# Kernel optimization log

Hardware: AMD Instinct MI355X
Metric: run time of the kernel (lower is better)

## Reference

```python
import jax, jax.numpy as jnp
import numpy as np

# SmallViT config (reconstructed; see shape_source)
B, C, H, W = 1024, 3, 32, 32
P = 4                # patch size
D = 128              # embed dim
NH, DH = 4, 32       # heads, head dim
FF = 256             # mlp hidden
L = 4                # encoder layers
T = (H // P) * (W // P) + 1  # 65 tokens
NQ = 4               # qubits
EPS = 1e-5


def layer_norm(x, s, b):
    m = x.mean(-1, keepdims=True)
    v = ((x - m) ** 2).mean(-1, keepdims=True)
    return (x - m) * jax.lax.rsqrt(v + EPS) * s + b


def setup_inputs() -> dict:
    key = jax.random.key(0)
    ks = iter(jax.random.split(key, 32))
    w = lambda *shape: jax.random.normal(next(ks), shape, jnp.float32) * 0.02
    inp = {
        'x': jax.random.normal(next(ks), (B, C, H, W), jnp.float32),
        'patch_w': w(D, C, P, P),
        'patch_b': jnp.zeros((D,), jnp.float32),
        'cls_token': w(1, 1, D),
        'pos_embed': w(1, T, D),
        # stacked per-layer encoder params (torch Linear convention: [out,in])
        'qkv_w': w(L, 3 * D, D), 'qkv_b': jnp.zeros((L, 3 * D), jnp.float32),
        'out_w': w(L, D, D),     'out_b': jnp.zeros((L, D), jnp.float32),
        'ln1_s': jnp.ones((L, D), jnp.float32), 'ln1_b': jnp.zeros((L, D), jnp.float32),
        'ln2_s': jnp.ones((L, D), jnp.float32), 'ln2_b': jnp.zeros((L, D), jnp.float32),
        'ff1_w': w(L, FF, D), 'ff1_b': jnp.zeros((L, FF), jnp.float32),
        'ff2_w': w(L, D, FF), 'ff2_b': jnp.zeros((L, D), jnp.float32),
        # quantum_reduce: Linear(128,32) -> ReLU -> Linear(32,4)
        'qr1_w': w(32, D), 'qr1_b': jnp.zeros((32,), jnp.float32),
        'qr2_w': w(NQ, 32), 'qr2_b': jnp.zeros((NQ,), jnp.float32),
        'q_weights': jax.random.normal(next(ks), (NQ,), jnp.float32),
        'clf_w': w(10, D + NQ), 'clf_b': jnp.zeros((10,), jnp.float32),
    }
    return inp


def reference(x, patch_w, patch_b, cls_token, pos_embed,
              qkv_w, qkv_b, out_w, out_b, ln1_s, ln1_b, ln2_s, ln2_b,
              ff1_w, ff1_b, ff2_w, ff2_b,
              qr1_w, qr1_b, qr2_w, qr2_b, q_weights, clf_w, clf_b):
    b = x.shape[0]
    # patch embed: conv stride==kernel -> reshape + einsum
    xp = x.reshape(b, C, H // P, P, W // P, P)
    tok = jnp.einsum('bcipjq,dcpq->bijd', xp, patch_w).reshape(b, -1, D) + patch_b
    # prepend cls, add pos
    h = jnp.concatenate([jnp.broadcast_to(cls_token, (b, 1, D)), tok], axis=1) + pos_embed
    scale = 1.0 / np.sqrt(DH)
    for i in range(L):
        # self-attention (post-LN encoder layer)
        qkv = h @ qkv_w[i].T + qkv_b[i]                      # [b,T,3D]
        q, k, v = jnp.split(qkv, 3, axis=-1)
        q = q.reshape(b, T, NH, DH).transpose(0, 2, 1, 3)
        k = k.reshape(b, T, NH, DH).transpose(0, 2, 1, 3)
        v = v.reshape(b, T, NH, DH).transpose(0, 2, 1, 3)
        attn = jax.nn.softmax(jnp.einsum('bhqd,bhkd->bhqk', q, k) * scale, axis=-1)
        o = jnp.einsum('bhqk,bhkd->bhqd', attn, v).transpose(0, 2, 1, 3).reshape(b, T, D)
        o = o @ out_w[i].T + out_b[i]
        h = layer_norm(h + o, ln1_s[i], ln1_b[i])
        ff = jax.nn.relu(h @ ff1_w[i].T + ff1_b[i]) @ ff2_w[i].T + ff2_b[i]
        h = layer_norm(h + ff, ln2_s[i], ln2_b[i])
    cls_out = h[:, 0]                                         # [b,D]
    q_in = jnp.tanh(jax.nn.relu(cls_out @ qr1_w.T + qr1_b) @ qr2_w.T + qr2_b)  # [b,4]
    # closed-form 4-qubit circuit: RY(in) RX(w) + CNOT chain -> <Z_i> = cumprod cos(in)cos(w)
    q_out = jnp.cumprod(jnp.cos(q_in) * jnp.cos(q_weights)[None, :], axis=-1)
    combined = jnp.concatenate([cls_out, q_out], axis=1)      # [b,132]
    return combined @ clf_w.T + clf_b                         # [b,10]
```

## Files before the change

kernel.cpp:

```cpp
#include <hip/hip_runtime.h>

typedef unsigned short ushort_t;
typedef unsigned int   uint32;
typedef short s16x8 __attribute__((ext_vector_type(8)));
typedef float f32x4 __attribute__((ext_vector_type(4)));

#define HS    136
#define KOF   0
#define VOF   9248
#define SLOF  18464
#define BIGN  29344
#define EPS_  1e-5f
#define SCALE2_ 0.25503483f

#define MFMA16(a,b,c) __builtin_amdgcn_mfma_f32_16x16x32_bf16((a),(b),(c),0,0,0)

__device__ __forceinline__ float bfu(ushort_t u) {
  union { uint32 i; float f; } c; c.i = ((uint32)u) << 16; return c.f;
}
__device__ __forceinline__ void bf2(uint32 u, float& a, float& b) {
  union { uint32 i; float f; } c0, c1;
  c0.i = u << 16; c1.i = u & 0xffff0000u; a = c0.f; b = c1.f;
}
__device__ __forceinline__ ushort_t f2bf(float f) {
  union { float f; uint32 i; } c; c.f = f;
  uint32 r = c.i + 0x7fffu + ((c.i >> 16) & 1u);
  return (ushort_t)(r >> 16);
}

__device__ bool sniff_f32(const ushort_t* x) {
  int insane = 0, zeros = 0;
  for (int i = 0; i < 256; ++i) {
    ushort_t u = x[i];
    int e = (u >> 7) & 0xFF;
    if (u == 0) zeros++;
    else if (e == 0xFF || e < 0x60) insane++;
  }
  return (insane >= 16) || (zeros >= 64);
}

struct WPack {
  const void* src[23];
  unsigned    off[23];
  unsigned    n[23];
};

__global__ __launch_bounds__(256) void canon(WPack p, const ushort_t* x, ushort_t* dst,
                                             int* flagOut) {
  const bool f32 = sniff_f32(x);
  const int gid = blockIdx.x * blockDim.x + threadIdx.x;
  const int gsz = gridDim.x * blockDim.x;
  for (int a = 0; a < 23; ++a) {
    unsigned n = p.n[a];
    ushort_t* d = dst + p.off[a];
    if (f32) {
      const float* s = (const float*)p.src[a];
      for (unsigned i = gid; i < n; i += gsz) d[i] = f2bf(s[i]);
    } else {
      const ushort_t* s = (const ushort_t*)p.src[a];
      for (unsigned i = gid; i < n; i += gsz) d[i] = s[i];
    }
  }
  if (blockIdx.x == 0 && threadIdx.x == 0) *flagOut = f32 ? 1 : 0;
}

__global__ __launch_bounds__(320, 2)
void vit_fused(const ushort_t* __restrict__ x,
               const ushort_t* __restrict__ patch_w,
               const ushort_t* __restrict__ patch_b,
               const ushort_t* __restrict__ cls_token,
               const ushort_t* __restrict__ pos_embed,
               const ushort_t* __restrict__ qkv_w,
               const ushort_t* __restrict__ qkv_b,
               const ushort_t* __restrict__ out_w,
               const ushort_t* __restrict__ out_b,
               const ushort_t* __restrict__ ln1_s,
               const ushort_t* __restrict__ ln1_b,
               const ushort_t* __restrict__ ln2_s,
               const ushort_t* __restrict__ ln2_b,
               const ushort_t* __restrict__ ff1_w,
               const ushort_t* __restrict__ ff1_b,
               const ushort_t* __restrict__ ff2_w,
               const ushort_t* __restrict__ ff2_b,
               const ushort_t* __restrict__ qr1_w,
               const ushort_t* __restrict__ qr1_b,
               const ushort_t* __restrict__ qr2_w,
               const ushort_t* __restrict__ qr2_b,
               const ushort_t* __restrict__ q_weights,
               const ushort_t* __restrict__ clf_w,
               const ushort_t* __restrict__ clf_b,
               const int* __restrict__ flag,
               void* __restrict__ out)
{
  __shared__ __align__(16) ushort_t h_s[80 * HS];
  __shared__ __align__(16) ushort_t big[BIGN];

  const int tid  = threadIdx.x;
  const int wid  = tid >> 6;
  const int lane = tid & 63;
  const int lr   = lane & 15;
  const int lq   = lane >> 4;
  const int b    = blockIdx.x;
  const bool f32m = (*flag != 0);
  const int m0 = wid * 16;

  uint32* bx = (uint32*)big;
  if (f32m) {
    const float* xf = (const float*)x + (size_t)b * 3072;
    for (int i = tid; i < 1536; i += 320) {
      uint32 lo = f2bf(xf[2 * i]);
      uint32 hi = f2bf(xf[2 * i + 1]);
      bx[i] = lo | (hi << 16);
    }
  } else {
    const uint32* xb = (const uint32*)x + (size_t)b * 1536;
    for (int i = tid; i < 1536; i += 320) bx[i] = xb[i];
  }
  {
    const uint32* pw = (const uint32*)patch_w;
    for (int i = tid; i < 3072; i += 320) bx[1536 + i] = pw[i];
  }
  __syncthreads();

  #pragma unroll 1
  for (int idx = tid; idx < 8192; idx += 320) {
    int p = idx >> 7, d = idx & 127;
    int pi = p >> 3, pj = p & 7;
    float acc = 0.f;
    #pragma unroll
    for (int c = 0; c < 3; ++c) {
      #pragma unroll
      for (int py = 0; py < 4; ++py) {
        const uint32* xr = bx + ((c * 1024 + (pi * 4 + py) * 32 + pj * 4) >> 1);
        const uint32* wr = bx + 1536 + ((d * 48 + c * 16 + py * 4) >> 1);
        #pragma unroll
        for (int q2 = 0; q2 < 2; ++q2) {
          float xa, xb2, wa, wb;
          bf2(xr[q2], xa, xb2); bf2(wr[q2], wa, wb);
          acc += xa * wa + xb2 * wb;
        }
      }
    }
    acc += bfu(patch_b[d]) + bfu(pos_embed[(1 + p) * 128 + d]);
    h_s[(1 + p) * HS + d] = f2bf(acc);
  }
  if (tid < 128) h_s[tid] = f2bf(bfu(cls_token[tid]) + bfu(pos_embed[tid]));
  for (int i = tid; i < 15 * HS; i += 320) h_s[65 * HS + i] = 0;

  #pragma unroll 1
  for (int il = 0; il < 4; ++il) {
    __syncthreads();

    const ushort_t* Wqkv = qkv_w + (size_t)il * 384 * 128;
    const ushort_t* Bqkv = qkv_b + il * 384;
    const ushort_t* Wo   = out_w + (size_t)il * 128 * 128;
    ushort_t* bw = big + SLOF + wid * 2176;

    #pragma unroll 2
    for (int u = wid * 16; u < wid * 16 + 16; ++u) {
      int ty = u & 1, r = u >> 1;
      int mt = r >> 3, nt = r & 7;
      int km0 = mt * 16;
      int rb = (ty ? 256 : 128) + nt * 16;
      float bv = bfu(Bqkv[rb + lr]);
      f32x4 acc = {bv, bv, bv, bv};
      #pragma unroll
      for (int kc = 0; kc < 4; ++kc) {
        s16x8 a  = *(const s16x8*)&h_s[(km0 + lr) * HS + kc * 32 + lq * 8];
        s16x8 bb = *(const s16x8*)&Wqkv[(rb + lr) * 128 + kc * 32 + lq * 8];
        acc = MFMA16(a, bb, acc);
      }
      if (!ty) {
        #pragma unroll
        for (int i = 0; i < 4; ++i) {
          int row = km0 + lq * 4 + i;
          if (row < 68) big[KOF + row * 136 + nt * 16 + lr] = f2bf(acc[i]);
        }
      } else {
        int tk = km0 + lq * 4;
        if (tk < 68) {
          uint32 w0 = (uint32)f2bf(acc[0]) | ((uint32)f2bf(acc[1]) << 16);
          uint32 w1 = (uint32)f2bf(acc[2]) | ((uint32)f2bf(acc[3]) << 16);
          uint32* dst = (uint32*)&big[VOF + (nt * 16 + lr) * 72 + tk];
          dst[0] = w0; dst[1] = w1;
        }
      }
    }
    __syncthreads();

    {
      s16x8 ha[4];
      #pragma unroll
      for (int kc = 0; kc < 4; ++kc)
        ha[kc] = *(const s16x8*)&h_s[(m0 + lr) * HS + kc * 32 + lq * 8];
      f32x4 opA[8];
      #pragma unroll
      for (int nt = 0; nt < 8; ++nt) {
        float bv = bfu(out_b[il * 128 + nt * 16 + lr]);
        opA[nt] = (f32x4){bv, bv, bv, bv};
      }
      #pragma unroll 1
      for (int ih = 0; ih < 4; ++ih) {
        #pragma unroll
        for (int n2 = 0; n2 < 2; ++n2) {
          int rb = ih * 32 + n2 * 16;
          float bv = bfu(Bqkv[rb + lr]);
          f32x4 acc = {bv, bv, bv, bv};
          #pragma unroll
          for (int kc = 0; kc < 4; ++kc) {
            s16x8 bb = *(const s16x8*)&Wqkv[(rb + lr) * 128 + kc * 32 + lq * 8];
            acc = MFMA16(ha[kc], bb, acc);
          }
          #pragma unroll
          for (int i = 0; i < 4; ++i)
            bw[(lq * 4 + i) * 40 + n2 * 16 + lr] = f2bf(acc[i] * SCALE2_);
        }
        s16x8 aq = *(const s16x8*)&bw[lr * 40 + lq * 8];
        f32x4 S[5];
        #pragma unroll
        for (int jt = 0; jt < 5; ++jt) {
          s16x8 bb = *(const s16x8*)&big[KOF + (jt * 16 + lr) * 136 + ih * 32 + lq * 8];
          f32x4 z = {0.f, 0.f, 0.f, 0.f};
          S[jt] = MFMA16(aq, bb, z);
        }
        float mx[4] = {-1e30f, -1e30f, -1e30f, -1e30f};
        #pragma unroll
        for (int jt = 0; jt < 5; ++jt)
          #pragma unroll
          for (int i = 0; i < 4; ++i) {
            float sv = S[jt][i];
            if (jt == 4 && lr > 0) sv = -1e30f;
            S[jt][i] = sv;
            mx[i] = fmaxf(mx[i], sv);
          }
        #pragma unroll
        for (int off = 1; off < 16; off <<= 1)
          #pragma unroll
          for (int i = 0; i < 4; ++i) mx[i] = fmaxf(mx[i], __shfl_xor(mx[i], off));
        float sm[4] = {0.f, 0.f, 0.f, 0.f};
        #pragma unroll
        for (int jt = 0; jt < 5; ++jt)
          #pragma unroll
          for (int i = 0; i < 4; ++i) {
            float pv = exp2f(S[jt][i] - mx[i]);
            S[jt][i] = pv; sm[i] += pv;
          }
        #pragma unroll
        for (int off = 1; off < 16; off <<= 1)
          #pragma unroll
          for (int i = 0; i < 4; ++i) sm[i] += __shfl_xor(sm[i], off);
        float inv[4];
        #pragma unroll
        for (int i = 0; i < 4; ++i) inv[i] = 1.f / sm[i];
        #pragma unroll
        for (int i = 0; i < 4; ++i)
          #pragma unroll
          for (int jt = 0; jt < 4; ++jt)
            bw[(lq * 4 + i) * 72 + jt * 16 + lr] = f2bf(S[jt][i] * inv[i]);
        f32x4 ov[2];
        #pragma unroll
        for (int n2 = 0; n2 < 2; ++n2) {
          f32x4 acc = {0.f, 0.f, 0.f, 0.f};
          #pragma unroll
          for (int kc = 0; kc < 2; ++kc) {
            s16x8 a  = *(const s16x8*)&bw[lr * 72 + kc * 32 + lq * 8];
            s16x8 bb = *(const s16x8*)&big[VOF + (ih * 32 + n2 * 16 + lr) * 72 + kc * 32 + lq * 8];
            acc = MFMA16(a, bb, acc);
          }
          float v64 = bfu(big[VOF + (ih * 32 + n2 * 16 + lr) * 72 + 64]);
          #pragma unroll
          for (int i = 0; i < 4; ++i) {
            float p64 = __shfl(S[4][i], lane & 48) * inv[i];
            acc[i] += p64 * v64;
          }
          ov[n2] = acc;
        }
        #pragma unroll
        for (int n2 = 0; n2 < 2; ++n2)
          #pragma unroll
          for (int i = 0; i < 4; ++i)
            bw[(lq * 4 + i) * 40 + n2 * 16 + lr] = f2bf(ov[n2][i]);
        s16x8 ao = *(const s16x8*)&bw[lr * 40 + lq * 8];
        #pragma unroll
        for (int nt = 0; nt < 8; ++nt) {
          s16x8 bb = *(const s16x8*)&Wo[(nt * 16 + lr) * 128 + ih * 32 + lq * 8];
          opA[nt] = MFMA16(ao, bb, opA[nt]);
        }
      }

      float sv[4] = {0, 0, 0, 0}, ssv[4] = {0, 0, 0, 0};
      #pragma unroll
      for (int nt = 0; nt < 8; ++nt)
        #pragma unroll
        for (int i = 0; i < 4; ++i) {
          float r = opA[nt][i] + bfu(h_s[(m0 + lq * 4 + i) * HS + nt * 16 + lr]);
          opA[nt][i] = r; sv[i] += r; ssv[i] += r * r;
        }
      #pragma unroll
      for (int off = 1; off < 16; off <<= 1)
        #pragma unroll
        for (int i = 0; i < 4; ++i) {
          sv[i]  += __shfl_xor(sv[i], off);
          ssv[i] += __shfl_xor(ssv[i], off);
        }
      float mean[4], inv2[4];
      #pragma unroll
      for (int i = 0; i < 4; ++i) {
        mean[i] = sv[i] * (1.f / 128.f);
        inv2[i] = rsqrtf(fmaxf(ssv[i] * (1.f / 128.f) - mean[i] * mean[i], 0.f) + EPS_);
      }
      #pragma unroll
      for (int nt = 0; nt < 8; ++nt) {
        float g  = bfu(ln1_s[il * 128 + nt * 16 + lr]);
        float be = bfu(ln1_b[il * 128 + nt * 16 + lr]);
        #pragma unroll
        for (int i = 0; i < 4; ++i)
          h_s[(m0 + lq * 4 + i) * HS + nt * 16 + lr] =
              f2bf((opA[nt][i] - mean[i]) * inv2[i] * g + be);
      }

      const ushort_t* W1 = ff1_w + (size_t)il * 256 * 128;
      const ushort_t* W2 = ff2_w + (size_t)il * 128 * 256;
      s16x8 hf[4];
      #pragma unroll
      for (int kc = 0; kc < 4; ++kc)
        hf[kc] = *(const s16x8*)&h_s[(m0 + lr) * HS + kc * 32 + lq * 8];
      f32x4 acc2[8];
      #pragma unroll
      for (int nt = 0; nt < 8; ++nt) {
        float bv = bfu(ff2_b[il * 128 + nt * 16 + lr]);
        acc2[nt] = (f32x4){bv, bv, bv, bv};
      }
      #pragma unroll 1
      for (int half = 0; half < 2; ++half) {
        #pragma unroll 2
        for (int n8 = 0; n8 < 8; ++n8) {
          int ng = half * 8 + n8;
          float bv = bfu(ff1_b[il * 256 + ng * 16 + lr]);
          f32x4 acc = {bv, bv, bv, bv};
          #pragma unroll
          for (int kc = 0; kc < 4; ++kc) {
            s16x8 bb = *(const s16x8*)&W1[(ng * 16 + lr) * 128 + kc * 32 + lq * 8];
            acc = MFMA16(hf[kc], bb, acc);
          }
          #pragma unroll
          for (int i = 0; i < 4; ++i)
            bw[(lq * 4 + i) * 136 + n8 * 16 + lr] = f2bf(fmaxf(acc[i], 0.f));
        }
        #pragma unroll
        for (int kc = 0; kc < 4; ++kc) {
          s16x8 a2 = *(const s16x8*)&bw[lr * 136 + kc * 32 + lq * 8];
          #pragma unroll
          for (int nt = 0; nt < 8; ++nt) {
            s16x8 bb = *(const s16x8*)&W2[(nt * 16 + lr) * 256 + half * 128 + kc * 32 + lq * 8];
            acc2[nt] = MFMA16(a2, bb, acc2[nt]);
          }
        }
      }
      float s2[4] = {0, 0, 0, 0}, ss2[4] = {0, 0, 0, 0};
      #pragma unroll
      for (int nt = 0; nt < 8; ++nt)
        #pragma unroll
        for (int i = 0; i < 4; ++i) {
          float r = acc2[nt][i] + bfu(h_s[(m0 + lq * 4 + i) * HS + nt * 16 + lr]);
          acc2[nt][i] = r; s2[i] += r; ss2[i] += r * r;
        }
      #pragma unroll
      for (int off = 1; off < 16; off <<= 1)
        #pragma unroll
        for (int i = 0; i < 4; ++i) {
          s2[i]  += __shfl_xor(s2[i], off);
          ss2[i] += __shfl_xor(ss2[i], off);
        }
      float mean2[4], invb[4];
      #pragma unroll
      for (int i = 0; i < 4; ++i) {
        mean2[i] = s2[i] * (1.f / 128.f);
        invb[i]  = rsqrtf(fmaxf(ss2[i] * (1.f / 128.f) - mean2[i] * mean2[i], 0.f) + EPS_);
      }
      #pragma unroll
      for (int nt = 0; nt < 8; ++nt) {
        float g  = bfu(ln2_s[il * 128 + nt * 16 + lr]);
        float be = bfu(ln2_b[il * 128 + nt * 16 + lr]);
        #pragma unroll
        for (int i = 0; i < 4; ++i)
          h_s[(m0 + lq * 4 + i) * HS + nt * 16 + lr] =
              f2bf((acc2[nt][i] - mean2[i]) * invb[i] * g + be);
      }
    }
  }

  __syncthreads();
  float* scr = (float*)big;
  {
    int j = tid & 31;
    const uint32* hrow0 = (const uint32*)h_s;
    const uint32* w = (const uint32*)qr1_w + j * 64;
    float acc = 0.f;
    #pragma unroll 4
    for (int k2 = 0; k2 < 64; ++k2) {
      float ha, hb, wa, wb;
      bf2(hrow0[k2], ha, hb); bf2(w[k2], wa, wb);
      acc += ha * wa + hb * wb;
    }
    float u = fmaxf(acc + bfu(qr1_b[j]), 0.f);
    if (tid < 32) scr[tid] = u;
  }
  __syncthreads();
  if (tid < 10) {
    float qo[4]; float cp = 1.f;
    #pragma unroll
    for (int j2 = 0; j2 < 4; ++j2) {
      float acc = 0.f;
      #pragma unroll
      for (int k = 0; k < 32; ++k) acc += scr[k] * bfu(qr2_w[j2 * 32 + k]);
      float qin = tanhf(acc + bfu(qr2_b[j2]));
      cp *= cosf(qin) * cosf(bfu(q_weights[j2]));
      qo[j2] = cp;
    }
    const uint32* hrow0 = (const uint32*)h_s;
    const uint32* cw = (const uint32*)clf_w + tid * 66;
    float acc = 0.f;
    #pragma unroll 4
    for (int k2 = 0; k2 < 64; ++k2) {
      float ha, hb, wa, wb;
      bf2(hrow0[k2], ha, hb); bf2(cw[k2], wa, wb);
      acc += ha * wa + hb * wb;
    }
    #pragma unroll
    for (int d = 0; d < 4; ++d) acc += qo[d] * bfu(clf_w[tid * 132 + 128 + d]);
    acc += bfu(clf_b[tid]);
    if (f32m) ((float*)out)[b * 10 + tid] = acc;
    else      ((ushort_t*)out)[b * 10 + tid] = f2bf(acc);
  }
}

extern "C" void kernel_launch(void* const* d_in, const int* in_sizes, int n_in,
                              void* d_out, int out_size, void* d_ws, size_t ws_size,
                              hipStream_t stream) {
  WPack p;
  unsigned cur = 0;
  for (int i = 0; i < 23; ++i) {
    p.src[i] = d_in[i + 1];
    p.off[i] = cur;
    p.n[i]   = (unsigned)in_sizes[i + 1];
    cur += (p.n[i] + 7u) & ~7u;
  }
  ushort_t* wsb = (ushort_t*)d_ws;
  unsigned flag_off = (cur * 2 + 3u) & ~3u;
  int* flagp = (int*)((char*)d_ws + flag_off);
  const ushort_t* x = (const ushort_t*)d_in[0];

  canon<<<dim3(128), dim3(256), 0, stream>>>(p, x, wsb, flagp);

  int B = out_size / 10;
  vit_fused<<<dim3(B), dim3(320), 0, stream>>>(
      x,
      wsb + p.off[0],  wsb + p.off[1],  wsb + p.off[2],  wsb + p.off[3],
      wsb + p.off[4],  wsb + p.off[5],  wsb + p.off[6],  wsb + p.off[7],
      wsb + p.off[8],  wsb + p.off[9],  wsb + p.off[10], wsb + p.off[11],
      wsb + p.off[12], wsb + p.off[13], wsb + p.off[14], wsb + p.off[15],
      wsb + p.off[16], wsb + p.off[17], wsb + p.off[18], wsb + p.off[19],
      wsb + p.off[20], wsb + p.off[21], wsb + p.off[22],
      flagp, d_out);
}
```

Baseline: 874.5 us.

## Split heads and FFN hidden across wave pairs with 640-thread blocks

Doubles the block from 5 to 10 waves. Each pair of waves shares one 16-row token tile: one wave handles heads 0-1 and FFN hidden half 0, the other handles heads 2-3 and hidden half 1. The second wave's partial out-projection and FF2 sums go through a new fp32 LDS exchange buffer and are added during the layernorm. This shortens the serial per-wave chain and raises the number of waves per CU. In exchange it needs more LDS (lower block occupancy), two extra barriers per layer, and leaves half the waves idle during the layernorms.

Measured after the change: 908.2 us. 3.9% more time.

```diff
diff --git a/kernel.cpp b/kernel.cpp
--- a/kernel.cpp
+++ b/kernel.cpp
@@ -9,7 +9,8 @@
 #define KOF   0
 #define VOF   9248
 #define SLOF  18464
-#define BIGN  29344
+#define EXOF  40224
+#define BIGN  61024
 #define EPS_  1e-5f
 #define SCALE2_ 0.25503483f
 
@@ -64,7 +65,7 @@
   if (blockIdx.x == 0 && threadIdx.x == 0) *flagOut = f32 ? 1 : 0;
 }
 
-__global__ __launch_bounds__(320, 2)
+__global__ __launch_bounds__(640, 3)
 void vit_fused(const ushort_t* __restrict__ x,
                const ushort_t* __restrict__ patch_w,
                const ushort_t* __restrict__ patch_b,
@@ -102,28 +103,33 @@
   const int lq   = lane >> 4;
   const int b    = blockIdx.x;
   const bool f32m = (*flag != 0);
-  const int m0 = wid * 16;
+  const int mt   = wid >> 1;
+  const int hg   = wid & 1;
+  const int m0   = mt * 16;
+
+  ushort_t* bw  = big + SLOF + wid * 2176;
+  float*    exf = (float*)&big[EXOF] + mt * 2080;
 
   uint32* bx = (uint32*)big;
   if (f32m) {
     const float* xf = (const float*)x + (size_t)b * 3072;
-    for (int i = tid; i < 1536; i += 320) {
+    for (int i = tid; i < 1536; i += 640) {
       uint32 lo = f2bf(xf[2 * i]);
       uint32 hi = f2bf(xf[2 * i + 1]);
       bx[i] = lo | (hi << 16);
     }
   } else {
     const uint32* xb = (const uint32*)x + (size_t)b * 1536;
-    for (int i = tid; i < 1536; i += 320) bx[i] = xb[i];
+    for (int i = tid; i < 1536; i += 640) bx[i] = xb[i];
   }
   {
     const uint32* pw = (const uint32*)patch_w;
-    for (int i = tid; i < 3072; i += 320) bx[1536 + i] = pw[i];
+    for (int i = tid; i < 3072; i += 640) bx[1536 + i] = pw[i];
   }
   __syncthreads();
 
   #pragma unroll 1
-  for (int idx = tid; idx < 8192; idx += 320) {
+  for (int idx = tid; idx < 8192; idx += 640) {
     int p = idx >> 7, d = idx & 127;
     int pi = p >> 3, pj = p & 7;
     float acc = 0.f;
@@ -145,7 +151,7 @@
     h_s[(1 + p) * HS + d] = f2bf(acc);
   }
   if (tid < 128) h_s[tid] = f2bf(bfu(cls_token[tid]) + bfu(pos_embed[tid]));
-  for (int i = tid; i < 15 * HS; i += 320) h_s[65 * HS + i] = 0;
+  for (int i = tid; i < 15 * HS; i += 640) h_s[65 * HS + i] = 0;
 
   #pragma unroll 1
   for (int il = 0; il < 4; ++il) {
@@ -154,13 +160,12 @@
     const ushort_t* Wqkv = qkv_w + (size_t)il * 384 * 128;
     const ushort_t* Bqkv = qkv_b + il * 384;
     const ushort_t* Wo   = out_w + (size_t)il * 128 * 128;
-    ushort_t* bw = big + SLOF + wid * 2176;
 
     #pragma unroll 2
-    for (int u = wid * 16; u < wid * 16 + 16; ++u) {
+    for (int u = wid * 8; u < wid * 8 + 8; ++u) {
       int ty = u & 1, r = u >> 1;
-      int mt = r >> 3, nt = r & 7;
-      int km0 = mt * 16;
+      int kmt = r >> 3, nt = r & 7;
+      int km0 = kmt * 16;
       int rb = (ty ? 256 : 128) + nt * 16;
       float bv = bfu(Bqkv[rb + lr]);
       f32x4 acc = {bv, bv, bv, bv};
@@ -188,19 +193,20 @@
     }
     __syncthreads();
 
+    f32x4 opA[8];
+    #pragma unroll
+    for (int nt = 0; nt < 8; ++nt) {
+      float bv = (hg == 0) ? bfu(out_b[il * 128 + nt * 16 + lr]) : 0.f;
+      opA[nt] = (f32x4){bv, bv, bv, bv};
+    }
     {
       s16x8 ha[4];
       #pragma unroll
       for (int kc = 0; kc < 4; ++kc)
         ha[kc] = *(const s16x8*)&h_s[(m0 + lr) * HS + kc * 32 + lq * 8];
-      f32x4 opA[8];
-      #pragma unroll
-      for (int nt = 0; nt < 8; ++nt) {
-        float bv = bfu(out_b[il * 128 + nt * 16 + lr]);
-        opA[nt] = (f32x4){bv, bv, bv, bv};
-      }
       #pragma unroll 1
-      for (int ih = 0; ih < 4; ++ih) {
+      for (int hh = 0; hh < 2; ++hh) {
+        int ih = hg * 2 + hh;
         #pragma unroll
         for (int n2 = 0; n2 < 2; ++n2) {
           int rb = ih * 32 + n2 * 16;
@@ -287,13 +293,23 @@
           opA[nt] = MFMA16(ao, bb, opA[nt]);
         }
       }
-
+    }
+    if (hg == 1) {
+      #pragma unroll
+      for (int nt = 0; nt < 8; ++nt)
+        #pragma unroll
+        for (int i = 0; i < 4; ++i)
+          exf[(lq * 4 + i) * 130 + nt * 16 + lr] = opA[nt][i];
+    }
+    __syncthreads();
+    if (hg == 0) {
       float sv[4] = {0, 0, 0, 0}, ssv[4] = {0, 0, 0, 0};
       #pragma unroll
       for (int nt = 0; nt < 8; ++nt)
         #pragma unroll
         for (int i = 0; i < 4; ++i) {
-          float r = opA[nt][i] + bfu(h_s[(m0 + lq * 4 + i) * HS + nt * 16 + lr]);
+          float r = opA[nt][i] + exf[(lq * 4 + i) * 130 + nt * 16 + lr]
+                  + bfu(h_s[(m0 + lq * 4 + i) * HS + nt * 16 + lr]);
           opA[nt][i] = r; sv[i] += r; ssv[i] += r * r;
         }
       #pragma unroll
@@ -303,22 +319,22 @@
           sv[i]  += __shfl_xor(sv[i], off);
           ssv[i] += __shfl_xor(ssv[i], off);
         }
-      float mean[4], inv2[4];
-      #pragma unroll
-      for (int i = 0; i < 4; ++i) {
-        mean[i] = sv[i] * (1.f / 128.f);
-        inv2[i] = rsqrtf(fmaxf(ssv[i] * (1.f / 128.f) - mean[i] * mean[i], 0.f) + EPS_);
-      }
       #pragma unroll
       for (int nt = 0; nt < 8; ++nt) {
         float g  = bfu(ln1_s[il * 128 + nt * 16 + lr]);
         float be = bfu(ln1_b[il * 128 + nt * 16 + lr]);
         #pragma unroll
-        for (int i = 0; i < 4; ++i)
+        for (int i = 0; i < 4; ++i) {
+          float mean = sv[i] * (1.f / 128.f);
+          float iv   = rsqrtf(fmaxf(ssv[i] * (1.f / 128.f) - mean * mean, 0.f) + EPS_);
           h_s[(m0 + lq * 4 + i) * HS + nt * 16 + lr] =
-              f2bf((opA[nt][i] - mean[i]) * inv2[i] * g + be);
-      }
-
+              f2bf((opA[nt][i] - mean) * iv * g + be);
+        }
+      }
+    }
+    __syncthreads();
+
+    {
       const ushort_t* W1 = ff1_w + (size_t)il * 256 * 128;
       const ushort_t* W2 = ff2_w + (size_t)il * 128 * 256;
       s16x8 hf[4];
@@ -328,64 +344,69 @@
       f32x4 acc2[8];
       #pragma unroll
       for (int nt = 0; nt < 8; ++nt) {
-        float bv = bfu(ff2_b[il * 128 + nt * 16 + lr]);
+        float bv = (hg == 0) ? bfu(ff2_b[il * 128 + nt * 16 + lr]) : 0.f;
         acc2[nt] = (f32x4){bv, bv, bv, bv};
       }
-      #pragma unroll 1
-      for (int half = 0; half < 2; ++half) {
-        #pragma unroll 2
-        for (int n8 = 0; n8 < 8; ++n8) {
-          int ng = half * 8 + n8;
-          float bv = bfu(ff1_b[il * 256 + ng * 16 + lr]);
-          f32x4 acc = {bv, bv, bv, bv};
-          #pragma unroll
-          for (int kc = 0; kc < 4; ++kc) {
-            s16x8 bb = *(const s16x8*)&W1[(ng * 16 + lr) * 128 + kc * 32 + lq * 8];
-            acc = MFMA16(hf[kc], bb, acc);
-          }
+      #pragma unroll 2
+      for (int n8 = 0; n8 < 8; ++n8) {
+        int ng = hg * 8 + n8;
+        float bv = bfu(ff1_b[il * 256 + ng * 16 + lr]);
+        f32x4 acc = {bv, bv, bv, bv};
+        #pragma unroll
+        for (int kc = 0; kc < 4; ++kc) {
+          s16x8 bb = *(const s16x8*)&W1[(ng * 16 + lr) * 128 + kc * 32 + lq * 8];
+          acc = MFMA16(hf[kc], bb, acc);
+        }
+        #pragma unroll
+        for (int i = 0; i < 4; ++i)
+          bw[(lq * 4 + i) * 136 + n8 * 16 + lr] = f2bf(fmaxf(acc[i], 0.f));
+      }
+      #pragma unroll
+      for (int kc = 0; kc < 4; ++kc) {
+        s16x8 a2 = *(const s16x8*)&bw[lr * 136 + kc * 32 + lq * 8];
+        #pragma unroll
+        for (int nt = 0; nt < 8; ++nt) {
+          s16x8 bb = *(const s16x8*)&W2[(nt * 16 + lr) * 256 + hg * 128 + kc * 32 + lq * 8];
+          acc2[nt] = MFMA16(a2, bb, acc2[nt]);
+        }
+      }
+      if (hg == 1) {
+        #pragma unroll
+        for (int nt = 0; nt < 8; ++nt)
           #pragma unroll
           for (int i = 0; i < 4; ++i)
-            bw[(lq * 4 + i) * 136 + n8 * 16 + lr] = f2bf(fmaxf(acc[i], 0.f));
-        }
-        #pragma unroll
-        for (int kc = 0; kc < 4; ++kc) {
-          s16x8 a2 = *(const s16x8*)&bw[lr * 136 + kc * 32 + lq * 8];
-          #pragma unroll
-          for (int nt = 0; nt < 8; ++nt) {
-            s16x8 bb = *(const s16x8*)&W2[(nt * 16 + lr) * 256 + half * 128 + kc * 32 + lq * 8];
-            acc2[nt] = MFMA16(a2, bb, acc2[nt]);
-          }
-        }
-      }
-      float s2[4] = {0, 0, 0, 0}, ss2[4] = {0, 0, 0, 0};
-      #pragma unroll
-      for (int nt = 0; nt < 8; ++nt)
-        #pragma unroll
-        for (int i = 0; i < 4; ++i) {
-          float r = acc2[nt][i] + bfu(h_s[(m0 + lq * 4 + i) * HS + nt * 16 + lr]);
-          acc2[nt][i] = r; s2[i] += r; ss2[i] += r * r;
-        }
-      #pragma unroll
-      for (int off = 1; off < 16; off <<= 1)
-        #pragma unroll
-        for (int i = 0; i < 4; ++i) {
-          s2[i]  += __shfl_xor(s2[i], off);
-          ss2[i] += __shfl_xor(ss2[i], off);
-        }
-      float mean2[4], invb[4];
-      #pragma unroll
-      for (int i = 0; i < 4; ++i) {
-        mean2[i] = s2[i] * (1.f / 128.f);
-        invb[i]  = rsqrtf(fmaxf(ss2[i] * (1.f / 128.f) - mean2[i] * mean2[i], 0.f) + EPS_);
-      }
-      #pragma unroll
-      for (int nt = 0; nt < 8; ++nt) {
-        float g  = bfu(ln2_s[il * 128 + nt * 16 + lr]);
-        float be = bfu(ln2_b[il * 128 + nt * 16 + lr]);
-        #pragma unroll
-        for (int i = 0; i < 4; ++i)
-          h_s[(m0 + lq * 4 + i) * HS + nt * 16 + lr] =
-              f2bf((acc2[nt][i] - mean2[i]) * invb[i] * g + be);
+            exf[(lq * 4 + i) * 130 + nt * 16 + lr] = acc2[nt][i];
+      }
+      __syncthreads();
+      if (hg == 0) {
+        float sv[4] = {0, 0, 0, 0}, ssv[4] = {0, 0, 0, 0};
+        #pragma unroll
+        for (int nt = 0; nt < 8; ++nt)
+          #pragma unroll
+          for (int i = 0; i < 4; ++i) {
+            float r = acc2[nt][i] + exf[(lq * 4 + i) * 130 + nt * 16 + lr]
+                    + bfu(h_s[(m0 + lq * 4 + i) * HS + nt * 16 + lr]);
+            acc2[nt][i] = r; sv[i] += r; ssv[i] += r * r;
+          }
+        #pragma unroll
+        for (int off = 1; off < 16; off <<= 1)
+          #pragma unroll
+          for (int i = 0; i < 4; ++i) {
+            sv[i]  += __shfl_xor(sv[i], off);
+            ssv[i] += __shfl_xor(ssv[i], off);
+          }
+        #pragma unroll
+        for (int nt = 0; nt < 8; ++nt) {
+          float g  = bfu(ln2_s[il * 128 + nt * 16 + lr]);
+          float be = bfu(ln2_b[il * 128 + nt * 16 + lr]);
+          #pragma unroll
+          for (int i = 0; i < 4; ++i) {
+            float mean = sv[i] * (1.f / 128.f);
+            float iv   = rsqrtf(fmaxf(ssv[i] * (1.f / 128.f) - mean * mean, 0.f) + EPS_);
+            h_s[(m0 + lq * 4 + i) * HS + nt * 16 + lr] =
+                f2bf((acc2[nt][i] - mean) * iv * g + be);
+          }
+        }
       }
     }
   }
@@ -454,7 +475,7 @@
   canon<<<dim3(128), dim3(256), 0, stream>>>(p, x, wsb, flagp);
 
   int B = out_size / 10;
-  vit_fused<<<dim3(B), dim3(320), 0, stream>>>(
+  vit_fused<<<dim3(B), dim3(640), 0, stream>>>(
       x,
       wsb + p.off[0],  wsb + p.off[1],  wsb + p.off[2],  wsb + p.off[3],
       wsb + p.off[4],  wsb + p.off[5],  wsb + p.off[6],  wsb + p.off[7],
```

## Split fused per-image ViT kernel into per-stage batched GEMM kernels

Applied to the files above, without the earlier changes.

Replaces the single per-image fused kernel with a pipeline of separate kernels for patch embed, QKV projection, attention, output projection with LayerNorm, FF1 and FF2 with LayerNorm, and the head. Intermediate activations now go through workspace buffers in global memory. Each GEMM tiles 64 rows across images, and weights are staged in shared memory once per block, so per-block weight reloads and the low occupancy of the large monolithic block go away. In exchange it adds many launches and extra global memory traffic for the intermediates. The old fused kernel is kept as a fallback when the workspace is too small or B is not a multiple of 64.

Result: faster. 724.3 us (-17.2%).

```diff
diff --git a/kernel.cpp b/kernel.cpp
--- a/kernel.cpp
+++ b/kernel.cpp
@@ -5,14 +5,8 @@
 typedef short s16x8 __attribute__((ext_vector_type(8)));
 typedef float f32x4 __attribute__((ext_vector_type(4)));
 
-#define HS    136
-#define KOF   0
-#define VOF   9248
-#define SLOF  18464
-#define BIGN  29344
 #define EPS_  1e-5f
 #define SCALE2_ 0.25503483f
-
 #define MFMA16(a,b,c) __builtin_amdgcn_mfma_f32_16x16x32_bf16((a),(b),(c),0,0,0)
 
 __device__ __forceinline__ float bfu(ushort_t u) {
@@ -64,46 +58,443 @@
   if (blockIdx.x == 0 && threadIdx.x == 0) *flagOut = f32 ? 1 : 0;
 }
 
+
+__global__ __launch_bounds__(256)
+void k_patch(const ushort_t* __restrict__ x, const ushort_t* __restrict__ patch_w,
+             const ushort_t* __restrict__ patch_b, const ushort_t* __restrict__ cls_token,
+             const ushort_t* __restrict__ pos_embed, const int* __restrict__ flag,
+             ushort_t* __restrict__ hbuf) {
+  __shared__ uint32 bx[4608];
+  const int tid = threadIdx.x, b = blockIdx.x;
+  const bool f32m = (*flag != 0);
+  if (f32m) {
+    const float* xf = (const float*)x + (size_t)b * 3072;
+    for (int i = tid; i < 1536; i += 256) {
+      uint32 lo = f2bf(xf[2 * i]);
+      uint32 hi = f2bf(xf[2 * i + 1]);
+      bx[i] = lo | (hi << 16);
+    }
+  } else {
+    const uint32* xb = (const uint32*)x + (size_t)b * 1536;
+    for (int i = tid; i < 1536; i += 256) bx[i] = xb[i];
+  }
+  {
+    const uint32* pw = (const uint32*)patch_w;
+    for (int i = tid; i < 3072; i += 256) bx[1536 + i] = pw[i];
+  }
+  __syncthreads();
+  #pragma unroll 1
+  for (int it = 0; it < 32; ++it) {
+    int idx = tid + 256 * it;
+    int p = idx >> 7, d = idx & 127;
+    int pi = p >> 3, pj = p & 7;
+    float acc = 0.f;
+    #pragma unroll
+    for (int c = 0; c < 3; ++c)
+      #pragma unroll
+      for (int py = 0; py < 4; ++py) {
+        const uint32* xr = bx + ((c * 1024 + (pi * 4 + py) * 32 + pj * 4) >> 1);
+        const uint32* wr = bx + 1536 + ((d * 48 + c * 16 + py * 4) >> 1);
+        #pragma unroll
+        for (int q2 = 0; q2 < 2; ++q2) {
+          float xa, xb2, wa, wb;
+          bf2(xr[q2], xa, xb2); bf2(wr[q2], wa, wb);
+          acc += xa * wa + xb2 * wb;
+        }
+      }
+    acc += bfu(patch_b[d]) + bfu(pos_embed[(1 + p) * 128 + d]);
+    hbuf[((size_t)b * 65 + 1 + p) * 128 + d] = f2bf(acc);
+  }
+  if (tid < 128)
+    hbuf[(size_t)b * 65 * 128 + tid] = f2bf(bfu(cls_token[tid]) + bfu(pos_embed[tid]));
+}
+
+__global__ __launch_bounds__(256)
+void k_qkv(const ushort_t* __restrict__ hbuf, const ushort_t* __restrict__ W,
+           const ushort_t* __restrict__ bias, ushort_t* __restrict__ qb,
+           ushort_t* __restrict__ kb, ushort_t* __restrict__ vtb) {
+  __shared__ __align__(16) ushort_t Bs[64 * 136];
+  const int tid = threadIdx.x, wid = tid >> 6, lane = tid & 63;
+  const int lr = lane & 15, lq = lane >> 4;
+  const int bm = blockIdx.x, nc = blockIdx.y;
+  {
+    const uint32* Wd = (const uint32*)W;
+    uint32* Bd = (uint32*)Bs;
+    for (int i = tid; i < 4096; i += 256) {
+      int row = i >> 6, cw = i & 63;
+      Bd[row * 68 + cw] = Wd[(nc * 64 + row) * 64 + cw];
+    }
+  }
+  __syncthreads();
+  const int r0 = bm * 64 + wid * 16;
+  s16x8 a[4];
+  #pragma unroll
+  for (int kc = 0; kc < 4; ++kc)
+    a[kc] = *(const s16x8*)&hbuf[(size_t)(r0 + lr) * 128 + kc * 32 + lq * 8];
+  #pragma unroll
+  for (int nt = 0; nt < 4; ++nt) {
+    int c0 = nc * 64 + nt * 16;
+    float bv = bfu(bias[c0 + lr]);
+    f32x4 acc = {bv, bv, bv, bv};
+    #pragma unroll
+    for (int kc = 0; kc < 4; ++kc) {
+      s16x8 bb = *(const s16x8*)&Bs[(nt * 16 + lr) * 136 + kc * 32 + lq * 8];
+      acc = MFMA16(a[kc], bb, acc);
+    }
+    int c = c0 + lr;
+    #pragma unroll
+    for (int i = 0; i < 4; ++i) {
+      int r = r0 + lq * 4 + i;
+      int b = r / 65, t = r - b * 65;
+      if (c0 < 128) {
+        int h = c >> 5, d = c & 31;
+        qb[((size_t)(b * 4 + h) * 80 + t) * 32 + d] = f2bf(acc[i] * SCALE2_);
+      } else if (c0 < 256) {
+        int c2 = c - 128;
+        kb[((size_t)(b * 4 + (c2 >> 5)) * 80 + t) * 32 + (c2 & 31)] = f2bf(acc[i]);
+      } else {
+        int c2 = c - 256;
+        vtb[((size_t)(b * 4 + (c2 >> 5)) * 32 + (c2 & 31)) * 80 + t] = f2bf(acc[i]);
+      }
+    }
+  }
+}
+
+__global__ __launch_bounds__(64)
+void k_attn(const ushort_t* __restrict__ qb, const ushort_t* __restrict__ kb,
+            const ushort_t* __restrict__ vtb, ushort_t* __restrict__ obuf) {
+  __shared__ __align__(16) ushort_t ks[80 * 40];
+  __shared__ __align__(16) ushort_t vs[32 * 96];
+  __shared__ __align__(16) ushort_t ps[16 * 96];
+  const int lane = threadIdx.x;
+  const int lr = lane & 15, lq = lane >> 4;
+  const int bh = blockIdx.x;
+  {
+    const uint32* kd = (const uint32*)(kb + (size_t)bh * 2560);
+    uint32* kls = (uint32*)ks;
+    #pragma unroll
+    for (int it = 0; it < 20; ++it) {
+      int u = it * 64 + lane;
+      kls[(u >> 4) * 20 + (u & 15)] = kd[u];
+    }
+    const uint32* vd = (const uint32*)(vtb + (size_t)bh * 2560);
+    uint32* vls = (uint32*)vs;
+    #pragma unroll
+    for (int it = 0; it < 20; ++it) {
+      int u = it * 64 + lane;
+      vls[(u / 40) * 48 + (u % 40)] = vd[u];
+    }
+    for (int u = lane; u < 512; u += 64)
+      vs[(u >> 4) * 96 + 80 + (u & 15)] = 0;
+  }
+  __syncthreads();
+  const int b = bh >> 2, h = bh & 3;
+  #pragma unroll 1
+  for (int mt = 0; mt < 5; ++mt) {
+    s16x8 aq = *(const s16x8*)&qb[((size_t)bh * 80 + mt * 16 + lr) * 32 + lq * 8];
+    f32x4 S[5];
+    #pragma unroll
+    for (int jt = 0; jt < 5; ++jt) {
+      s16x8 bb = *(const s16x8*)&ks[(jt * 16 + lr) * 40 + lq * 8];
+      f32x4 z = {0.f, 0.f, 0.f, 0.f};
+      S[jt] = MFMA16(aq, bb, z);
+    }
+    float mx[4] = {-1e30f, -1e30f, -1e30f, -1e30f};
+    #pragma unroll
+    for (int jt = 0; jt < 5; ++jt)
+      #pragma unroll
+      for (int i = 0; i < 4; ++i) {
+        float sv = S[jt][i];
+        if (jt == 4 && lr > 0) sv = -1e30f;
+        S[jt][i] = sv;
+        mx[i] = fmaxf(mx[i], sv);
+      }
+    #pragma unroll
+    for (int off = 1; off < 16; off <<= 1)
+      #pragma unroll
+      for (int i = 0; i < 4; ++i) mx[i] = fmaxf(mx[i], __shfl_xor(mx[i], off));
+    float sm[4] = {0.f, 0.f, 0.f, 0.f};
+    #pragma unroll
+    for (int jt = 0; jt < 5; ++jt)
+      #pragma unroll
+      for (int i = 0; i < 4; ++i) {
+        float pv = exp2f(S[jt][i] - mx[i]);
+        S[jt][i] = pv; sm[i] += pv;
+      }
+    #pragma unroll
+    for (int off = 1; off < 16; off <<= 1)
+      #pragma unroll
+      for (int i = 0; i < 4; ++i) sm[i] += __shfl_xor(sm[i], off);
+    float inv[4];
+    #pragma unroll
+    for (int i = 0; i < 4; ++i) inv[i] = 1.f / sm[i];
+    #pragma unroll
+    for (int i = 0; i < 4; ++i) {
+      #pragma unroll
+      for (int jt = 0; jt < 5; ++jt)
+        ps[(lq * 4 + i) * 96 + jt * 16 + lr] = f2bf(S[jt][i] * inv[i]);
+      ps[(lq * 4 + i) * 96 + 80 + lr] = 0;
+    }
+    #pragma unroll
+    for (int n2 = 0; n2 < 2; ++n2) {
+      f32x4 acc = {0.f, 0.f, 0.f, 0.f};
+      #pragma unroll
+      for (int kc = 0; kc < 3; ++kc) {
+        s16x8 a  = *(const s16x8*)&ps[lr * 96 + kc * 32 + lq * 8];
+        s16x8 bb = *(const s16x8*)&vs[(n2 * 16 + lr) * 96 + kc * 32 + lq * 8];
+        acc = MFMA16(a, bb, acc);
+      }
+      #pragma unroll
+      for (int i = 0; i < 4; ++i) {
+        int t = mt * 16 + lq * 4 + i;
+        if (t < 65)
+          obuf[((size_t)b * 65 + t) * 128 + h * 32 + n2 * 16 + lr] = f2bf(acc[i]);
+      }
+    }
+  }
+}
+
+__global__ __launch_bounds__(256)
+void k_out_ln(const ushort_t* __restrict__ obuf, const ushort_t* __restrict__ Wo,
+              const ushort_t* __restrict__ ob, const ushort_t* __restrict__ g,
+              const ushort_t* __restrict__ be, ushort_t* __restrict__ hbuf) {
+  __shared__ __align__(16) ushort_t Bs[128 * 136];
+  const int tid = threadIdx.x, wid = tid >> 6, lane = tid & 63;
+  const int lr = lane & 15, lq = lane >> 4;
+  const int bm = blockIdx.x;
+  {
+    const uint32* Wd = (const uint32*)Wo;
+    uint32* Bd = (uint32*)Bs;
+    for (int i = tid; i < 8192; i += 256)
+      Bd[(i >> 6) * 68 + (i & 63)] = Wd[i];
+  }
+  __syncthreads();
+  const int r0 = bm * 64 + wid * 16;
+  s16x8 a[4];
+  #pragma unroll
+  for (int kc = 0; kc < 4; ++kc)
+    a[kc] = *(const s16x8*)&obuf[(size_t)(r0 + lr) * 128 + kc * 32 + lq * 8];
+  float xr[8][4];
+  float sv[4] = {0, 0, 0, 0}, ssv[4] = {0, 0, 0, 0};
+  #pragma unroll
+  for (int nt = 0; nt < 8; ++nt) {
+    float bv = bfu(ob[nt * 16 + lr]);
+    f32x4 acc = {bv, bv, bv, bv};
+    #pragma unroll
+    for (int kc = 0; kc < 4; ++kc) {
+      s16x8 bb = *(const s16x8*)&Bs[(nt * 16 + lr) * 136 + kc * 32 + lq * 8];
+      acc = MFMA16(a[kc], bb, acc);
+    }
+    #pragma unroll
+    for (int i = 0; i < 4; ++i) {
+      float r = acc[i] + bfu(hbuf[(size_t)(r0 + lq * 4 + i) * 128 + nt * 16 + lr]);
+      xr[nt][i] = r; sv[i] += r; ssv[i] += r * r;
+    }
+  }
+  #pragma unroll
+  for (int off = 1; off < 16; off <<= 1)
+    #pragma unroll
+    for (int i = 0; i < 4; ++i) {
+      sv[i]  += __shfl_xor(sv[i], off);
+      ssv[i] += __shfl_xor(ssv[i], off);
+    }
+  #pragma unroll
+  for (int nt = 0; nt < 8; ++nt) {
+    float gg = bfu(g[nt * 16 + lr]);
+    float bb = bfu(be[nt * 16 + lr]);
+    #pragma unroll
+    for (int i = 0; i < 4; ++i) {
+      float mean = sv[i] * (1.f / 128.f);
+      float iv = rsqrtf(fmaxf(ssv[i] * (1.f / 128.f) - mean * mean, 0.f) + EPS_);
+      hbuf[(size_t)(r0 + lq * 4 + i) * 128 + nt * 16 + lr] =
+          f2bf((xr[nt][i] - mean) * iv * gg + bb);
+    }
+  }
+}
+
+__global__ __launch_bounds__(256)
+void k_ff1(const ushort_t* __restrict__ hbuf, const ushort_t* __restrict__ W1,
+           const ushort_t* __restrict__ b1, ushort_t* __restrict__ fbuf) {
+  __shared__ __align__(16) ushort_t Bs[64 * 136];
+  const int tid = threadIdx.x, wid = tid >> 6, lane = tid & 63;
+  const int lr = lane & 15, lq = lane >> 4;
+  const int bm = blockIdx.x, nc = blockIdx.y;
+  {
+    const uint32* Wd = (const uint32*)W1;
+    uint32* Bd = (uint32*)Bs;
+    for (int i = tid; i < 4096; i += 256) {
+      int row = i >> 6, cw = i & 63;
+      Bd[row * 68 + cw] = Wd[(nc * 64 + row) * 64 + cw];
+    }
+  }
+  __syncthreads();
+  const int r0 = bm * 64 + wid * 16;
+  s16x8 a[4];
+  #pragma unroll
+  for (int kc = 0; kc < 4; ++kc)
+    a[kc] = *(const s16x8*)&hbuf[(size_t)(r0 + lr) * 128 + kc * 32 + lq * 8];
+  #pragma unroll
+  for (int nt = 0; nt < 4; ++nt) {
+    int c0 = nc * 64 + nt * 16;
+    float bv = bfu(b1[c0 + lr]);
+    f32x4 acc = {bv, bv, bv, bv};
+    #pragma unroll
+    for (int kc = 0; kc < 4; ++kc) {
+      s16x8 bb = *(const s16x8*)&Bs[(nt * 16 + lr) * 136 + kc * 32 + lq * 8];
+      acc = MFMA16(a[kc], bb, acc);
+    }
+    #pragma unroll
+    for (int i = 0; i < 4; ++i)
+      fbuf[(size_t)(r0 + lq * 4 + i) * 256 + c0 + lr] = f2bf(fmaxf(acc[i], 0.f));
+  }
+}
+
+__global__ __launch_bounds__(256)
+void k_ff2_ln(const ushort_t* __restrict__ fbuf, const ushort_t* __restrict__ W2,
+              const ushort_t* __restrict__ b2, const ushort_t* __restrict__ g,
+              const ushort_t* __restrict__ be, ushort_t* __restrict__ hbuf) {
+  __shared__ __align__(16) ushort_t Bs[128 * 136];
+  const int tid = threadIdx.x, wid = tid >> 6, lane = tid & 63;
+  const int lr = lane & 15, lq = lane >> 4;
+  const int bm = blockIdx.x;
+  const int r0 = bm * 64 + wid * 16;
+  f32x4 acc2[8];
+  #pragma unroll
+  for (int nt = 0; nt < 8; ++nt) {
+    float bv = bfu(b2[nt * 16 + lr]);
+    acc2[nt] = (f32x4){bv, bv, bv, bv};
+  }
+  #pragma unroll 1
+  for (int half = 0; half < 2; ++half) {
+    {
+      const uint32* Wd = (const uint32*)W2;
+      uint32* Bd = (uint32*)Bs;
+      for (int i = tid; i < 8192; i += 256) {
+        int row = i >> 6, cw = i & 63;
+        Bd[row * 68 + cw] = Wd[row * 128 + half * 64 + cw];
+      }
+    }
+    __syncthreads();
+    s16x8 a[4];
+    #pragma unroll
+    for (int kc = 0; kc < 4; ++kc)
+      a[kc] = *(const s16x8*)&fbuf[(size_t)(r0 + lr) * 256 + half * 128 + kc * 32 + lq * 8];
+    #pragma unroll
+    for (int nt = 0; nt < 8; ++nt)
+      #pragma unroll
+      for (int kc = 0; kc < 4; ++kc) {
+        s16x8 bb = *(const s16x8*)&Bs[(nt * 16 + lr) * 136 + kc * 32 + lq * 8];
+        acc2[nt] = MFMA16(a[kc], bb, acc2[nt]);
+      }
+    __syncthreads();
+  }
+  float sv[4] = {0, 0, 0, 0}, ssv[4] = {0, 0, 0, 0};
+  #pragma unroll
+  for (int nt = 0; nt < 8; ++nt)
+    #pragma unroll
+    for (int i = 0; i < 4; ++i) {
+      float r = acc2[nt][i] + bfu(hbuf[(size_t)(r0 + lq * 4 + i) * 128 + nt * 16 + lr]);
+      acc2[nt][i] = r; sv[i] += r; ssv[i] += r * r;
+    }
+  #pragma unroll
+  for (int off = 1; off < 16; off <<= 1)
+    #pragma unroll
+    for (int i = 0; i < 4; ++i) {
+      sv[i]  += __shfl_xor(sv[i], off);
+      ssv[i] += __shfl_xor(ssv[i], off);
+    }
+  #pragma unroll
+  for (int nt = 0; nt < 8; ++nt) {
+    float gg = bfu(g[nt * 16 + lr]);
+    float bb = bfu(be[nt * 16 + lr]);
+    #pragma unroll
+    for (int i = 0; i < 4; ++i) {
+      float mean = sv[i] * (1.f / 128.f);
+      float iv = rsqrtf(fmaxf(ssv[i] * (1.f / 128.f) - mean * mean, 0.f) + EPS_);
+      hbuf[(size_t)(r0 + lq * 4 + i) * 128 + nt * 16 + lr] =
+          f2bf((acc2[nt][i] - mean) * iv * gg + bb);
+    }
+  }
+}
+
+__global__ __launch_bounds__(64)
+void k_head(const ushort_t* __restrict__ hbuf, const ushort_t* __restrict__ qr1_w,
+            const ushort_t* __restrict__ qr1_b, const ushort_t* __restrict__ qr2_w,
+            const ushort_t* __restrict__ qr2_b, const ushort_t* __restrict__ q_weights,
+            const ushort_t* __restrict__ clf_w, const ushort_t* __restrict__ clf_b,
+            const int* __restrict__ flag, void* __restrict__ out) {
+  __shared__ float scr[32];
+  const int lane = threadIdx.x, b = blockIdx.x;
+  const bool f32m = (*flag != 0);
+  const uint32* hrow0 = (const uint32*)(hbuf + (size_t)b * 65 * 128);
+  {
+    int j = lane & 31;
+    const uint32* w = (const uint32*)qr1_w + j * 64;
+    float acc = 0.f;
+    #pragma unroll 4
+    for (int k2 = 0; k2 < 64; ++k2) {
+      float ha, hb, wa, wb;
+      bf2(hrow0[k2], ha, hb); bf2(w[k2], wa, wb);
+      acc += ha * wa + hb * wb;
+    }
+    if (lane < 32) scr[lane] = fmaxf(acc + bfu(qr1_b[j]), 0.f);
+  }
+  __syncthreads();
+  if (lane < 10) {
+    float qo[4]; float cp = 1.f;
+    #pragma unroll
+    for (int j2 = 0; j2 < 4; ++j2) {
+      float acc = 0.f;
+      #pragma unroll
+      for (int k = 0; k < 32; ++k) acc += scr[k] * bfu(qr2_w[j2 * 32 + k]);
+      float qin = tanhf(acc + bfu(qr2_b[j2]));
+      cp *= cosf(qin) * cosf(bfu(q_weights[j2]));
+      qo[j2] = cp;
+    }
+    const uint32* cw = (const uint32*)clf_w + lane * 66;
+    float acc = 0.f;
+    #pragma unroll 4
+    for (int k2 = 0; k2 < 64; ++k2) {
+      float ha, hb, wa, wb;
+      bf2(hrow0[k2], ha, hb); bf2(cw[k2], wa, wb);
+      acc += ha * wa + hb * wb;
+    }
+    #pragma unroll
+    for (int d = 0; d < 4; ++d) acc += qo[d] * bfu(clf_w[lane * 132 + 128 + d]);
+    acc += bfu(clf_b[lane]);
+    if (f32m) ((float*)out)[b * 10 + lane] = acc;
+    else      ((ushort_t*)out)[b * 10 + lane] = f2bf(acc);
+  }
+}
+
+#define HS    136
+#define KOF   0
+#define VOF   9248
+#define SLOF  18464
+#define BIGN  29344
+
 __global__ __launch_bounds__(320, 2)
-void vit_fused(const ushort_t* __restrict__ x,
-               const ushort_t* __restrict__ patch_w,
-               const ushort_t* __restrict__ patch_b,
-               const ushort_t* __restrict__ cls_token,
-               const ushort_t* __restrict__ pos_embed,
-               const ushort_t* __restrict__ qkv_w,
-               const ushort_t* __restrict__ qkv_b,
-               const ushort_t* __restrict__ out_w,
-               const ushort_t* __restrict__ out_b,
-               const ushort_t* __restrict__ ln1_s,
-               const ushort_t* __restrict__ ln1_b,
-               const ushort_t* __restrict__ ln2_s,
-               const ushort_t* __restrict__ ln2_b,
-               const ushort_t* __restrict__ ff1_w,
-               const ushort_t* __restrict__ ff1_b,
-               const ushort_t* __restrict__ ff2_w,
-               const ushort_t* __restrict__ ff2_b,
-               const ushort_t* __restrict__ qr1_w,
-               const ushort_t* __restrict__ qr1_b,
-               const ushort_t* __restrict__ qr2_w,
-               const ushort_t* __restrict__ qr2_b,
-               const ushort_t* __restrict__ q_weights,
-               const ushort_t* __restrict__ clf_w,
-               const ushort_t* __restrict__ clf_b,
-               const int* __restrict__ flag,
-               void* __restrict__ out)
+void vit_mono(const ushort_t* __restrict__ x, const ushort_t* __restrict__ patch_w,
+              const ushort_t* __restrict__ patch_b, const ushort_t* __restrict__ cls_token,
+              const ushort_t* __restrict__ pos_embed, const ushort_t* __restrict__ qkv_w,
+              const ushort_t* __restrict__ qkv_b, const ushort_t* __restrict__ out_w,
+              const ushort_t* __restrict__ out_b, const ushort_t* __restrict__ ln1_s,
+              const ushort_t* __restrict__ ln1_b, const ushort_t* __restrict__ ln2_s,
+              const ushort_t* __restrict__ ln2_b, const ushort_t* __restrict__ ff1_w,
+              const ushort_t* __restrict__ ff1_b, const ushort_t* __restrict__ ff2_w,
+              const ushort_t* __restrict__ ff2_b, const ushort_t* __restrict__ qr1_w,
+              const ushort_t* __restrict__ qr1_b, const ushort_t* __restrict__ qr2_w,
+              const ushort_t* __restrict__ qr2_b, const ushort_t* __restrict__ q_weights,
+              const ushort_t* __restrict__ clf_w, const ushort_t* __restrict__ clf_b,
+              const int* __restrict__ flag, void* __restrict__ out)
 {
   __shared__ __align__(16) ushort_t h_s[80 * HS];
   __shared__ __align__(16) ushort_t big[BIGN];
-
-  const int tid  = threadIdx.x;
-  const int wid  = tid >> 6;
-  const int lane = tid & 63;
-  const int lr   = lane & 15;
-  const int lq   = lane >> 4;
-  const int b    = blockIdx.x;
+  const int tid = threadIdx.x, wid = tid >> 6, lane = tid & 63;
+  const int lr = lane & 15, lq = lane >> 4;
+  const int b = blockIdx.x;
   const bool f32m = (*flag != 0);
   const int m0 = wid * 16;
-
   uint32* bx = (uint32*)big;
   if (f32m) {
     const float* xf = (const float*)x + (size_t)b * 3072;
@@ -116,19 +507,16 @@
     const uint32* xb = (const uint32*)x + (size_t)b * 1536;
     for (int i = tid; i < 1536; i += 320) bx[i] = xb[i];
   }
-  {
-    const uint32* pw = (const uint32*)patch_w;
-    for (int i = tid; i < 3072; i += 320) bx[1536 + i] = pw[i];
-  }
+  { const uint32* pw = (const uint32*)patch_w;
+    for (int i = tid; i < 3072; i += 320) bx[1536 + i] = pw[i]; }
   __syncthreads();
-
   #pragma unroll 1
   for (int idx = tid; idx < 8192; idx += 320) {
     int p = idx >> 7, d = idx & 127;
     int pi = p >> 3, pj = p & 7;
     float acc = 0.f;
     #pragma unroll
-    for (int c = 0; c < 3; ++c) {
+    for (int c = 0; c < 3; ++c)
       #pragma unroll
       for (int py = 0; py < 4; ++py) {
         const uint32* xr = bx + ((c * 1024 + (pi * 4 + py) * 32 + pj * 4) >> 1);
@@ -140,22 +528,18 @@
           acc += xa * wa + xb2 * wb;
         }
       }
-    }
     acc += bfu(patch_b[d]) + bfu(pos_embed[(1 + p) * 128 + d]);
     h_s[(1 + p) * HS + d] = f2bf(acc);
   }
   if (tid < 128) h_s[tid] = f2bf(bfu(cls_token[tid]) + bfu(pos_embed[tid]));
   for (int i = tid; i < 15 * HS; i += 320) h_s[65 * HS + i] = 0;
-
   #pragma unroll 1
   for (int il = 0; il < 4; ++il) {
     __syncthreads();
-
     const ushort_t* Wqkv = qkv_w + (size_t)il * 384 * 128;
     const ushort_t* Bqkv = qkv_b + il * 384;
     const ushort_t* Wo   = out_w + (size_t)il * 128 * 128;
     ushort_t* bw = big + SLOF + wid * 2176;
-
     #pragma unroll 2
     for (int u = wid * 16; u < wid * 16 + 16; ++u) {
       int ty = u & 1, r = u >> 1;
@@ -187,7 +571,6 @@
       }
     }
     __syncthreads();
-
     {
       s16x8 ha[4];
       #pragma unroll
@@ -287,7 +670,6 @@
           opA[nt] = MFMA16(ao, bb, opA[nt]);
         }
       }
-
       float sv[4] = {0, 0, 0, 0}, ssv[4] = {0, 0, 0, 0};
       #pragma unroll
       for (int nt = 0; nt < 8; ++nt)
@@ -311,14 +693,13 @@
       }
       #pragma unroll
       for (int nt = 0; nt < 8; ++nt) {
-        float g  = bfu(ln1_s[il * 128 + nt * 16 + lr]);
+        float g = bfu(ln1_s[il * 128 + nt * 16 + lr]);
         float be = bfu(ln1_b[il * 128 + nt * 16 + lr]);
         #pragma unroll
         for (int i = 0; i < 4; ++i)
           h_s[(m0 + lq * 4 + i) * HS + nt * 16 + lr] =
               f2bf((opA[nt][i] - mean[i]) * inv2[i] * g + be);
       }
-
       const ushort_t* W1 = ff1_w + (size_t)il * 256 * 128;
       const ushort_t* W2 = ff2_w + (size_t)il * 128 * 256;
       s16x8 hf[4];
@@ -380,7 +761,7 @@
       }
       #pragma unroll
       for (int nt = 0; nt < 8; ++nt) {
-        float g  = bfu(ln2_s[il * 128 + nt * 16 + lr]);
+        float g = bfu(ln2_s[il * 128 + nt * 16 + lr]);
         float be = bfu(ln2_b[il * 128 + nt * 16 + lr]);
         #pragma unroll
         for (int i = 0; i < 4; ++i)
@@ -389,7 +770,6 @@
       }
     }
   }
-
   __syncthreads();
   float* scr = (float*)big;
   {
@@ -447,20 +827,53 @@
     cur += (p.n[i] + 7u) & ~7u;
   }
   ushort_t* wsb = (ushort_t*)d_ws;
-  unsigned flag_off = (cur * 2 + 3u) & ~3u;
-  int* flagp = (int*)((char*)d_ws + flag_off);
   const ushort_t* x = (const ushort_t*)d_in[0];
+  size_t wb = (size_t)cur * 2;
+  size_t fb = (wb + 3) & ~(size_t)3;
+  int* flagp = (int*)((char*)d_ws + fb);
 
   canon<<<dim3(128), dim3(256), 0, stream>>>(p, x, wsb, flagp);
 
   int B = out_size / 10;
-  vit_fused<<<dim3(B), dim3(320), 0, stream>>>(
-      x,
-      wsb + p.off[0],  wsb + p.off[1],  wsb + p.off[2],  wsb + p.off[3],
-      wsb + p.off[4],  wsb + p.off[5],  wsb + p.off[6],  wsb + p.off[7],
-      wsb + p.off[8],  wsb + p.off[9],  wsb + p.off[10], wsb + p.off[11],
-      wsb + p.off[12], wsb + p.off[13], wsb + p.off[14], wsb + p.off[15],
-      wsb + p.off[16], wsb + p.off[17], wsb + p.off[18], wsb + p.off[19],
-      wsb + p.off[20], wsb + p.off[21], wsb + p.off[22],
-      flagp, d_out);
-}
+  size_t HB = (size_t)B * 65 * 128 * 2;
+  size_t QB = (size_t)B * 4 * 80 * 32 * 2;
+  size_t hb = (fb + 4 + 255) & ~(size_t)255;
+  size_t qo = hb + HB, ko = qo + QB, vo = ko + QB, oo = vo + QB;
+  size_t need = oo + HB;
+  size_t FBYT = (size_t)B * 65 * 256 * 2;
+  bool pipe = (ws_size >= need) && (B % 64 == 0) && (FBYT <= 3 * QB);
+
+  #define WP(i) (wsb + p.off[i])
+  if (pipe) {
+    ushort_t* hbuf = (ushort_t*)((char*)d_ws + hb);
+    ushort_t* qb   = (ushort_t*)((char*)d_ws + qo);
+    ushort_t* kb   = (ushort_t*)((char*)d_ws + ko);
+    ushort_t* vtb  = (ushort_t*)((char*)d_ws + vo);
+    ushort_t* obuf = (ushort_t*)((char*)d_ws + oo);
+    ushort_t* fbuf = qb;
+    int MT = (B * 65) / 64;
+
+    k_patch<<<dim3(B), dim3(256), 0, stream>>>(x, WP(0), WP(1), WP(2), WP(3), flagp, hbuf);
+    for (int il = 0; il < 4; ++il) {
+      k_qkv<<<dim3(MT, 6), dim3(256), 0, stream>>>(
+          hbuf, WP(4) + (size_t)il * 49152, WP(5) + il * 384, qb, kb, vtb);
+      k_attn<<<dim3(B * 4), dim3(64), 0, stream>>>(qb, kb, vtb, obuf);
+      k_out_ln<<<dim3(MT), dim3(256), 0, stream>>>(
+          obuf, WP(6) + (size_t)il * 16384, WP(7) + il * 128,
+          WP(8) + il * 128, WP(9) + il * 128, hbuf);
+      k_ff1<<<dim3(MT, 4), dim3(256), 0, stream>>>(
+          hbuf, WP(12) + (size_t)il * 32768, WP(13) + il * 256, fbuf);
+      k_ff2_ln<<<dim3(MT), dim3(256), 0, stream>>>(
+          fbuf, WP(14) + (size_t)il * 32768, WP(15) + il * 128,
+          WP(10) + il * 128, WP(11) + il * 128, hbuf);
+    }
+    k_head<<<dim3(B), dim3(64), 0, stream>>>(
+        hbuf, WP(16), WP(17), WP(18), WP(19), WP(20), WP(21), WP(22), flagp, d_out);
+  } else {
+    vit_mono<<<dim3(B), dim3(320), 0, stream>>>(
+        x, WP(0), WP(1), WP(2), WP(3), WP(4), WP(5), WP(6), WP(7), WP(8), WP(9),
+        WP(10), WP(11), WP(12), WP(13), WP(14), WP(15), WP(16), WP(17), WP(18),
+        WP(19), WP(20), WP(21), WP(22), flagp, d_out);
+  }
+  #undef WP
+}
```
